# Kernel optimization log

Measured on AMD Instinct MI355X. Metric: run time of the kernel, lower is better.

The kernel has to match this reference:

```python
import jax, jax.numpy as jnp
import numpy as np
from math import sqrt

N_HEADS = 16

def setup_inputs() -> dict:
    key = jax.random.key(0)
    ks = jax.random.split(key, 6)
    B, T, C = 4, 2048, 1024
    s = 0.02
    return {
        "X": jax.random.normal(ks[0], (B, T, C), jnp.float32),
        "Wq": jax.random.normal(ks[1], (C, C), jnp.float32) * s,
        "Wk": jax.random.normal(ks[2], (C, C), jnp.float32) * s,
        "Wv": jax.random.normal(ks[3], (C, C), jnp.float32) * s,
        "Wo": jax.random.normal(ks[4], (C, C), jnp.float32) * s,
        "bo": jnp.zeros((C,), jnp.float32),
    }

def reference(X, Wq, Wk, Wv, Wo, bo):
    B, T, C = X.shape
    H = N_HEADS
    D = C // H
    scale = sqrt(C / H)  # == sqrt(D)
    # Linear layers (torch Linear: y = x @ W.T), split into heads: [B,H,T,D]
    Q = (X @ Wq.T).reshape(B, T, H, D).transpose(0, 2, 1, 3)
    K = (X @ Wk.T).reshape(B, T, H, D).transpose(0, 2, 1, 3)
    V = (X @ Wv.T).reshape(B, T, H, D).transpose(0, 2, 1, 3)
    A = jnp.einsum("bhtd,bhsd->bhts", Q, K) / scale  # [B,H,T,T]
    causal = jnp.tril(jnp.ones((T, T), dtype=bool))
    A = jnp.where(causal, A, -jnp.inf)
    A = jax.nn.softmax(A, axis=-1)
    Y = jnp.einsum("bhts,bhsd->bhtd", A, V)  # [B,H,T,D]
    Y = Y.transpose(0, 2, 1, 3).reshape(B, T, C)
    return Y @ Wo.T + bo
```

## Files before the change

### kernel.cpp

```cpp
#include <hip/hip_runtime.h>
#include <hip/hip_bf16.h>
#include <stdint.h>


typedef unsigned short u16;
typedef __attribute__((ext_vector_type(8))) __bf16 bf16x8;
typedef __attribute__((ext_vector_type(4))) float  f32x4;
typedef __attribute__((ext_vector_type(4))) unsigned short u16x4;
typedef __attribute__((ext_vector_type(4))) short s16x4;

#define B_  4
#define T_  2048
#define C_  1024
#define H_  16
#define D_  64
#define BT_ (B_ * T_)

#define Q_SCALE 0.1803368801111204f

__device__ __forceinline__ u16 f32_to_bf16(float f) {
    unsigned int u = __float_as_uint(f);
    unsigned int r = (u + 0x7FFFu + ((u >> 16) & 1u)) >> 16;
    return (u16)r;
}

__device__ __forceinline__ unsigned int pk_bf16(float a, float b) {
    float2 f2; f2.x = a; f2.y = b;
    __hip_bfloat162 h = __float22bfloat162_rn(f2);
    return *(unsigned int*)&h;
}

__device__ __forceinline__ void async16(const void* g, void* lds) {
    __builtin_amdgcn_global_load_lds(
        (const __attribute__((address_space(1))) void*)g,
        (__attribute__((address_space(3))) void*)lds, 16, 0, 0);
}

__global__ void cast_bf16_kernel(const float* __restrict__ in, u16* __restrict__ out, int n4) {
    int i = blockIdx.x * 256 + threadIdx.x;
    if (i >= n4) return;
    float4 v = ((const float4*)in)[i];
    u16x4 o;
    o[0] = f32_to_bf16(v.x); o[1] = f32_to_bf16(v.y);
    o[2] = f32_to_bf16(v.z); o[3] = f32_to_bf16(v.w);
    ((u16x4*)out)[i] = o;
}

__global__ void cast_w4_kernel(const float* __restrict__ w0, const float* __restrict__ w1,
                               const float* __restrict__ w2, const float* __restrict__ w3,
                               u16* __restrict__ o0, u16* __restrict__ o1,
                               u16* __restrict__ o2, u16* __restrict__ o3) {
    int which = blockIdx.y;
    const float* in = (which == 0) ? w0 : (which == 1) ? w1 : (which == 2) ? w2 : w3;
    u16* out = (which == 0) ? o0 : (which == 1) ? o1 : (which == 2) ? o2 : o3;
    int i = blockIdx.x * 256 + threadIdx.x;
    float4 v = ((const float4*)in)[i];
    u16x4 o;
    o[0] = f32_to_bf16(v.x); o[1] = f32_to_bf16(v.y);
    o[2] = f32_to_bf16(v.z); o[3] = f32_to_bf16(v.w);
    ((u16x4*)out)[i] = o;
}

__device__ __forceinline__ void gemm_core_128(
    const u16* __restrict__ A, const u16* __restrict__ B,
    u16* As, u16* Bs, int m0, int n0, f32x4 (&acc)[4][4])
{
    const int K = C_;
    int tid  = threadIdx.x;
    int lane = tid & 63, w = tid >> 6;
    int quad = lane >> 4, l15 = lane & 15;
    int wm = w >> 1, wn = w & 1;

    int c0 = tid, c1 = tid + 256;
    int row0 = c0 >> 2, row1 = c1 >> 2;
    int gc0 = (((c0 & 3) - (row0 >> 1)) & 3) * 8;
    int gc1 = (((c1 & 3) - (row1 >> 1)) & 3) * 8;
    int ldsb0 = (w * 64) * 16;
    int ldsb1 = (256 + w * 64) * 16;

    const u16* Arow0 = A + (m0 + row0) * K + gc0;
    const u16* Arow1 = A + (m0 + row1) * K + gc1;
    const u16* Brow0 = B + (n0 + row0) * K + gc0;
    const u16* Brow1 = B + (n0 + row1) * K + gc1;

    for (int kt = 0; kt < K / 32; ++kt) {
        int k0 = kt * 32;
        async16(Arow0 + k0, (char*)As + ldsb0);
        async16(Arow1 + k0, (char*)As + ldsb1);
        async16(Brow0 + k0, (char*)Bs + ldsb0);
        async16(Brow1 + k0, (char*)Bs + ldsb1);
        __syncthreads();

        bf16x8 a[4], b[4];
#pragma unroll
        for (int i = 0; i < 4; ++i) {
            int rA = wm * 64 + i * 16 + l15;
            a[i] = *(const bf16x8*)&As[rA * 32 + (((rA >> 1) + quad) & 3) * 8];
            int rB = wn * 64 + i * 16 + l15;
            b[i] = *(const bf16x8*)&Bs[rB * 32 + (((rB >> 1) + quad) & 3) * 8];
        }
#pragma unroll
        for (int i = 0; i < 4; ++i)
#pragma unroll
            for (int j = 0; j < 4; ++j)
                acc[i][j] = __builtin_amdgcn_mfma_f32_16x16x32_bf16(a[i], b[j], acc[i][j], 0, 0, 0);
        __syncthreads();
    }
}

__global__ __launch_bounds__(256, 4) void qkv_gemm(
    const u16* __restrict__ Xb,
    const u16* __restrict__ Wqb, const u16* __restrict__ Wkb, const u16* __restrict__ Wvb,
    u16* __restrict__ Qb, u16* __restrict__ Kb, u16* __restrict__ Vtb)
{
    __shared__ u16 As[128 * 32];
    __shared__ u16 Bs[128 * 32];
    int which = blockIdx.z;
    const u16* W = (which == 0) ? Wqb : ((which == 1) ? Wkb : Wvb);

    f32x4 acc[4][4];
    const f32x4 z4 = {0.f, 0.f, 0.f, 0.f};
#pragma unroll
    for (int i = 0; i < 4; ++i)
#pragma unroll
        for (int j = 0; j < 4; ++j) acc[i][j] = z4;

    int lane = threadIdx.x & 63, w = threadIdx.x >> 6;
    int quad = lane >> 4, l15 = lane & 15;
    int wm = w >> 1, wn = w & 1;

    if (which <= 1) {
        int m0 = blockIdx.x * 128, n0 = blockIdx.y * 128;
        gemm_core_128(W, Xb, As, Bs, m0, n0, acc);
        float s = (which == 0) ? Q_SCALE : 1.0f;
        u16* Out = (which == 0) ? Qb : Kb;
#pragma unroll
        for (int i = 0; i < 4; ++i) {
            int ch0 = m0 + wm * 64 + i * 16 + quad * 4;
#pragma unroll
            for (int j = 0; j < 4; ++j) {
                int t = n0 + wn * 64 + j * 16 + l15;
                u16x4 v;
#pragma unroll
                for (int r = 0; r < 4; ++r) v[r] = f32_to_bf16(acc[i][j][r] * s);
                *(u16x4*)&Out[(size_t)t * C_ + ch0] = v;
            }
        }
    } else {
        int m0 = blockIdx.y * 128, n0 = blockIdx.x * 128;
        gemm_core_128(Xb, W, As, Bs, m0, n0, acc);
#pragma unroll
        for (int i = 0; i < 4; ++i) {
            int t0 = m0 + wm * 64 + i * 16 + quad * 4;
#pragma unroll
            for (int j = 0; j < 4; ++j) {
                int col = n0 + wn * 64 + j * 16 + l15;
                int h = col >> 6, d = col & 63;
                u16x4 v;
#pragma unroll
                for (int r = 0; r < 4; ++r) v[r] = f32_to_bf16(acc[i][j][r]);
                int b = t0 >> 11, t = t0 & (T_ - 1);
                *(u16x4*)&Vtb[(((b * H_ + h) * D_ + d) * T_) + t] = v;
            }
        }
    }
}

__global__ __launch_bounds__(256) void attn_kernel(
    const u16* __restrict__ Qb, const u16* __restrict__ Kb,
    const u16* __restrict__ Vtb, u16* __restrict__ Yb)
{
    __shared__ u16 Ks0[64 * 64], Ks1[64 * 64];
    __shared__ u16 Vs0[64 * 64], Vs1[64 * 64];

    int id = blockIdx.x;
    int kk = id >> 8;
    int cc = id & 255;
    int jj = cc >> 6;
    int bh = cc & 63;
    int qt = (kk == 0) ? jj : (kk == 1) ? (15 - jj) : (kk == 2) ? (jj + 4) : (11 - jj);

    int tid = threadIdx.x, lane = tid & 63, w = tid >> 6;
    int quad = lane >> 4, l15 = lane & 15;
    int qbase = qt * 128;
    int b = bh >> 4, h = bh & 15;

    bf16x8 qf[2][2];
    {
        const u16* q0 = Qb + ((size_t)(b * T_ + qbase + w * 32 + l15)) * C_ + h * 64;
        qf[0][0] = *(const bf16x8*)(q0 + quad * 8);
        qf[0][1] = *(const bf16x8*)(q0 + 32 + quad * 8);
        const u16* q1 = q0 + 16 * C_;
        qf[1][0] = *(const bf16x8*)(q1 + quad * 8);
        qf[1][1] = *(const bf16x8*)(q1 + 32 + quad * 8);
    }

    int koff0[4], koff1[4], voff[4][4];
#pragma unroll
    for (int sblk = 0; sblk < 4; ++sblk) {
        int sr = sblk * 16 + l15;
        koff0[sblk] = (sr * 64 + ((quad + sr) & 7) * 8) * 2;
        koff1[sblk] = (sr * 64 + ((4 + quad + sr) & 7) * 8) * 2;
    }
#pragma unroll
    for (int n = 0; n < 4; ++n)
#pragma unroll
        for (int sblk = 0; sblk < 4; ++sblk) {
            int dr = n * 16 + l15;
            voff[n][sblk] = (dr * 64 + ((sblk * 2 + (quad >> 1) + dr) & 7) * 8 + (quad & 1) * 4) * 2;
        }

    float l_part[2] = {0.f, 0.f};
    f32x4 o_acc[2][4];
    const f32x4 z4 = {0.f, 0.f, 0.f, 0.f};
#pragma unroll
    for (int c = 0; c < 2; ++c)
#pragma unroll
        for (int n = 0; n < 4; ++n) o_acc[c][n] = z4;

    int cA = tid, cB = tid + 256;
    int sA = cA >> 3, sB = cB >> 3;
    int offA = (((cA & 7) - sA) & 7) * 8;
    int offB = (((cB & 7) - sB) & 7) * 8;
    const u16* Kbase = Kb + (size_t)(b * T_) * C_ + h * 64;
    const u16* Vbase = Vtb + (size_t)bh * D_ * T_;
    int ldsb0 = (w * 64) * 16, ldsb1 = (256 + w * 64) * 16;

    const int nst = 2 * qt + 2;

    const u16* kgpA = Kbase + (size_t)sA * C_ + offA;
    const u16* kgpB = Kbase + (size_t)sB * C_ + offB;
    const u16* vgpA = Vbase + sA * T_ + offA;
    const u16* vgpB = Vbase + sB * T_ + offB;

    async16(kgpA, (char*)Ks0 + ldsb0);
    async16(kgpB, (char*)Ks0 + ldsb1);
    async16(vgpA, (char*)Vs0 + ldsb0);
    async16(vgpB, (char*)Vs0 + ldsb1);
    kgpA += 64 * C_; kgpB += 64 * C_; vgpA += 64; vgpB += 64;

    auto tile_body = [&](int st, const u16* K_, const u16* V_, char* Kpf, char* Vpf) {
        __syncthreads();
        if (st + 1 < nst) {
            async16(kgpA, Kpf + ldsb0);
            async16(kgpB, Kpf + ldsb1);
            async16(vgpA, Vpf + ldsb0);
            async16(vgpB, Vpf + ldsb1);
        }
        kgpA += 64 * C_; kgpB += 64 * C_; vgpA += 64; vgpB += 64;

        f32x4 sv[2][4];
#pragma unroll
        for (int sblk = 0; sblk < 4; ++sblk) {
            bf16x8 k0 = *(const bf16x8*)((const char*)K_ + koff0[sblk]);
            bf16x8 k1 = *(const bf16x8*)((const char*)K_ + koff1[sblk]);
#pragma unroll
            for (int c = 0; c < 2; ++c) {
                f32x4 t0 = __builtin_amdgcn_mfma_f32_16x16x32_bf16(k0, qf[c][0], z4, 0, 0, 0);
                sv[c][sblk] = __builtin_amdgcn_mfma_f32_16x16x32_bf16(k1, qf[c][1], t0, 0, 0, 0);
            }
        }

        if (st >= 2 * qt) {
            int sb0 = st * 64 - qbase;
#pragma unroll
            for (int c = 0; c < 2; ++c) {
                int tl = w * 32 + c * 16 + l15;
#pragma unroll
                for (int sblk = 0; sblk < 4; ++sblk)
#pragma unroll
                    for (int r = 0; r < 4; ++r)
                        if (sb0 + sblk * 16 + quad * 4 + r > tl) sv[c][sblk][r] = -1e30f;
            }
        }

        s16x4 pfrag[2][4];
#pragma unroll
        for (int c = 0; c < 2; ++c) {
            f32x4 s4 = z4;
#pragma unroll
            for (int sblk = 0; sblk < 4; ++sblk) {
#pragma unroll
                for (int r = 0; r < 4; ++r)
                    sv[c][sblk][r] = __builtin_amdgcn_exp2f(sv[c][sblk][r]);
                s4 += sv[c][sblk];
                uint2 pk;
                pk.x = pk_bf16(sv[c][sblk][0], sv[c][sblk][1]);
                pk.y = pk_bf16(sv[c][sblk][2], sv[c][sblk][3]);
                pfrag[c][sblk] = *(s16x4*)&pk;
            }
            l_part[c] += (s4[0] + s4[1]) + (s4[2] + s4[3]);
        }

#pragma unroll
        for (int n = 0; n < 4; ++n)
#pragma unroll
            for (int sblk = 0; sblk < 4; ++sblk) {
                s16x4 va = *(const s16x4*)((const char*)V_ + voff[n][sblk]);
#pragma unroll
                for (int c = 0; c < 2; ++c)
                    o_acc[c][n] = __builtin_amdgcn_mfma_f32_16x16x16bf16_1k(va, pfrag[c][sblk], o_acc[c][n], 0, 0, 0);
            }
    };

    for (int st = 0; st < nst; st += 2) {
        tile_body(st,     Ks0, Vs0, (char*)Ks1, (char*)Vs1);
        tile_body(st + 1, Ks1, Vs1, (char*)Ks0, (char*)Vs0);
    }

#pragma unroll
    for (int c = 0; c < 2; ++c) {
        float l = l_part[c];
        l += __shfl_xor(l, 16, 64);
        l += __shfl_xor(l, 32, 64);
        float inv = 1.0f / l;
        int t = qbase + w * 32 + c * 16 + l15;
        size_t rowoff = ((size_t)b * T_ + t) * C_ + h * 64;
#pragma unroll
        for (int n = 0; n < 4; ++n) {
            uint2 pk;
            pk.x = pk_bf16(o_acc[c][n][0] * inv, o_acc[c][n][1] * inv);
            pk.y = pk_bf16(o_acc[c][n][2] * inv, o_acc[c][n][3] * inv);
            *(uint2*)&Yb[rowoff + n * 16 + quad * 4] = pk;
        }
    }
}

__global__ __launch_bounds__(256, 4) void proj_gemm(
    const u16* __restrict__ Yb, const u16* __restrict__ Wob,
    const float* __restrict__ bo, float* __restrict__ out)
{
    __shared__ u16 As[128 * 32];
    __shared__ u16 Bs[128 * 32];
    int m0 = blockIdx.x * 128, n0 = blockIdx.y * 128;

    f32x4 acc[4][4];
    const f32x4 z4 = {0.f, 0.f, 0.f, 0.f};
#pragma unroll
    for (int i = 0; i < 4; ++i)
#pragma unroll
        for (int j = 0; j < 4; ++j) acc[i][j] = z4;

    gemm_core_128(Wob, Yb, As, Bs, m0, n0, acc);

    int lane = threadIdx.x & 63, w = threadIdx.x >> 6;
    int quad = lane >> 4, l15 = lane & 15;
    int wm = w >> 1, wn = w & 1;

#pragma unroll
    for (int i = 0; i < 4; ++i) {
        int ch0 = m0 + wm * 64 + i * 16 + quad * 4;
        float4 b4 = *(const float4*)&bo[ch0];
#pragma unroll
        for (int j = 0; j < 4; ++j) {
            int t = n0 + wn * 64 + j * 16 + l15;
            float4 o;
            o.x = acc[i][j][0] + b4.x;
            o.y = acc[i][j][1] + b4.y;
            o.z = acc[i][j][2] + b4.z;
            o.w = acc[i][j][3] + b4.w;
            *(float4*)&out[(size_t)t * C_ + ch0] = o;
        }
    }
}

extern "C" void kernel_launch(void* const* d_in, const int* in_sizes, int n_in,
                              void* d_out, int out_size, void* d_ws, size_t ws_size,
                              hipStream_t stream) {
    const float* X  = (const float*)d_in[0];
    const float* Wq = (const float*)d_in[1];
    const float* Wk = (const float*)d_in[2];
    const float* Wv = (const float*)d_in[3];
    const float* Wo = (const float*)d_in[4];
    const float* bo = (const float*)d_in[5];

    char* ws = (char*)d_ws;
    u16* Xb  = (u16*)(ws);
    u16* Wqb = (u16*)(ws + (16u << 20));
    u16* Wkb = (u16*)(ws + (18u << 20));
    u16* Wvb = (u16*)(ws + (20u << 20));
    u16* Wob = (u16*)(ws + (22u << 20));
    u16* Qb  = (u16*)(ws + (24u << 20));
    u16* Kb  = (u16*)(ws + (40u << 20));
    u16* Vtb = (u16*)(ws + (56u << 20));
    u16* Yb  = (u16*)(ws + (72u << 20));

    cast_bf16_kernel<<<(BT_ * C_ / 4) / 256, 256, 0, stream>>>(X, Xb, BT_ * C_ / 4);
    cast_w4_kernel<<<dim3((C_ * C_ / 4) / 256, 4), 256, 0, stream>>>(
        Wq, Wk, Wv, Wo, Wqb, Wkb, Wvb, Wob);

    qkv_gemm<<<dim3(C_ / 128, BT_ / 128, 3), 256, 0, stream>>>(Xb, Wqb, Wkb, Wvb, Qb, Kb, Vtb);
    attn_kernel<<<dim3((T_ / 128) * B_ * H_), 256, 0, stream>>>(Qb, Kb, Vtb, Yb);
    proj_gemm<<<dim3(C_ / 128, BT_ / 128), 256, 0, stream>>>(Yb, Wob, bo, (float*)d_out);
}
```

Before: 264.6 us.

## Double-buffer GEMM LDS tiles and remap blocks for XCD-local reuse

The shared GEMM core now uses two LDS buffers, so the async global-to-LDS loads for the next K tile are issued while MFMAs run on the current tile. This removes one barrier per iteration and lets load latency overlap with compute. The QKV and projection GEMMs also switch to a 1D grid with a custom block-to-tile mapping, so the blocks placed on each XCD share rows of X/Y and get better L2 reuse. The cost is doubled LDS per block, which may lower occupancy, plus extra index arithmetic.

```diff
diff --git a/kernel.cpp b/kernel.cpp
--- a/kernel.cpp
+++ b/kernel.cpp
@@ -61,11 +61,12 @@
     ((u16x4*)out)[i] = o;
 }
 
-__device__ __forceinline__ void gemm_core_128(
+__device__ __forceinline__ void gemm_core_128_db(
     const u16* __restrict__ A, const u16* __restrict__ B,
     u16* As, u16* Bs, int m0, int n0, f32x4 (&acc)[4][4])
 {
     const int K = C_;
+    const int KT = K / 32;
     int tid  = threadIdx.x;
     int lane = tid & 63, w = tid >> 6;
     int quad = lane >> 4, l15 = lane & 15;
@@ -78,33 +79,51 @@
     int ldsb0 = (w * 64) * 16;
     int ldsb1 = (256 + w * 64) * 16;
 
-    const u16* Arow0 = A + (m0 + row0) * K + gc0;
-    const u16* Arow1 = A + (m0 + row1) * K + gc1;
-    const u16* Brow0 = B + (n0 + row0) * K + gc0;
-    const u16* Brow1 = B + (n0 + row1) * K + gc1;
-
-    for (int kt = 0; kt < K / 32; ++kt) {
-        int k0 = kt * 32;
-        async16(Arow0 + k0, (char*)As + ldsb0);
-        async16(Arow1 + k0, (char*)As + ldsb1);
-        async16(Brow0 + k0, (char*)Bs + ldsb0);
-        async16(Brow1 + k0, (char*)Bs + ldsb1);
+    const u16* ApA = A + (size_t)(m0 + row0) * K + gc0;
+    const u16* ApB = A + (size_t)(m0 + row1) * K + gc1;
+    const u16* BpA = B + (size_t)(n0 + row0) * K + gc0;
+    const u16* BpB = B + (size_t)(n0 + row1) * K + gc1;
+
+    char* As0 = (char*)As; char* As1 = (char*)As + 8192;
+    char* Bs0 = (char*)Bs; char* Bs1 = (char*)Bs + 8192;
+
+    int aoff[4], boff[4];
+#pragma unroll
+    for (int i = 0; i < 4; ++i) {
+        int rA = wm * 64 + i * 16 + l15;
+        aoff[i] = (rA * 32 + (((rA >> 1) + quad) & 3) * 8) * 2;
+        int rB = wn * 64 + i * 16 + l15;
+        boff[i] = (rB * 32 + (((rB >> 1) + quad) & 3) * 8) * 2;
+    }
+
+    async16(ApA, As0 + ldsb0); async16(ApB, As0 + ldsb1);
+    async16(BpA, Bs0 + ldsb0); async16(BpB, Bs0 + ldsb1);
+    ApA += 32; ApB += 32; BpA += 32; BpB += 32;
+
+    auto body = [&](int kt, const char* Ac, const char* Bc, char* Apf, char* Bpf) {
         __syncthreads();
+        if (kt + 1 < KT) {
+            async16(ApA, Apf + ldsb0); async16(ApB, Apf + ldsb1);
+            async16(BpA, Bpf + ldsb0); async16(BpB, Bpf + ldsb1);
+        }
+        ApA += 32; ApB += 32; BpA += 32; BpB += 32;
 
         bf16x8 a[4], b[4];
 #pragma unroll
         for (int i = 0; i < 4; ++i) {
-            int rA = wm * 64 + i * 16 + l15;
-            a[i] = *(const bf16x8*)&As[rA * 32 + (((rA >> 1) + quad) & 3) * 8];
-            int rB = wn * 64 + i * 16 + l15;
-            b[i] = *(const bf16x8*)&Bs[rB * 32 + (((rB >> 1) + quad) & 3) * 8];
+            a[i] = *(const bf16x8*)(Ac + aoff[i]);
+            b[i] = *(const bf16x8*)(Bc + boff[i]);
         }
 #pragma unroll
         for (int i = 0; i < 4; ++i)
 #pragma unroll
             for (int j = 0; j < 4; ++j)
                 acc[i][j] = __builtin_amdgcn_mfma_f32_16x16x32_bf16(a[i], b[j], acc[i][j], 0, 0, 0);
-        __syncthreads();
+    };
+
+    for (int kt = 0; kt < KT; kt += 2) {
+        body(kt,     As0, Bs0, As1, Bs1);
+        body(kt + 1, As1, Bs1, As0, Bs0);
     }
 }
 
@@ -113,9 +132,18 @@
     const u16* __restrict__ Wqb, const u16* __restrict__ Wkb, const u16* __restrict__ Wvb,
     u16* __restrict__ Qb, u16* __restrict__ Kb, u16* __restrict__ Vtb)
 {
-    __shared__ u16 As[128 * 32];
-    __shared__ u16 Bs[128 * 32];
-    int which = blockIdx.z;
+    __shared__ u16 As[2 * 128 * 32];
+    __shared__ u16 Bs[2 * 128 * 32];
+
+    int id = blockIdx.x;
+    int xcd = id & 7;
+    int local = id >> 3;
+    int yloc = local & 7;
+    int zx = local >> 3;
+    int bx = zx & 7;
+    int which = zx >> 3;
+    int by = xcd * 8 + yloc;
+
     const u16* W = (which == 0) ? Wqb : ((which == 1) ? Wkb : Wvb);
 
     f32x4 acc[4][4];
@@ -130,8 +158,8 @@
     int wm = w >> 1, wn = w & 1;
 
     if (which <= 1) {
-        int m0 = blockIdx.x * 128, n0 = blockIdx.y * 128;
-        gemm_core_128(W, Xb, As, Bs, m0, n0, acc);
+        int m0 = bx * 128, n0 = by * 128;
+        gemm_core_128_db(W, Xb, As, Bs, m0, n0, acc);
         float s = (which == 0) ? Q_SCALE : 1.0f;
         u16* Out = (which == 0) ? Qb : Kb;
 #pragma unroll
@@ -147,8 +175,8 @@
             }
         }
     } else {
-        int m0 = blockIdx.y * 128, n0 = blockIdx.x * 128;
-        gemm_core_128(Xb, W, As, Bs, m0, n0, acc);
+        int m0 = by * 128, n0 = bx * 128;
+        gemm_core_128_db(Xb, W, As, Bs, m0, n0, acc);
 #pragma unroll
         for (int i = 0; i < 4; ++i) {
             int t0 = m0 + wm * 64 + i * 16 + quad * 4;
@@ -330,9 +358,15 @@
     const u16* __restrict__ Yb, const u16* __restrict__ Wob,
     const float* __restrict__ bo, float* __restrict__ out)
 {
-    __shared__ u16 As[128 * 32];
-    __shared__ u16 Bs[128 * 32];
-    int m0 = blockIdx.x * 128, n0 = blockIdx.y * 128;
+    __shared__ u16 As[2 * 128 * 32];
+    __shared__ u16 Bs[2 * 128 * 32];
+
+    int id = blockIdx.x;
+    int xcd = id & 7;
+    int local = id >> 3;
+    int by = xcd * 8 + (local & 7);
+    int bx = local >> 3;
+    int m0 = bx * 128, n0 = by * 128;
 
     f32x4 acc[4][4];
     const f32x4 z4 = {0.f, 0.f, 0.f, 0.f};
@@ -341,7 +375,7 @@
 #pragma unroll
         for (int j = 0; j < 4; ++j) acc[i][j] = z4;
 
-    gemm_core_128(Wob, Yb, As, Bs, m0, n0, acc);
+    gemm_core_128_db(Wob, Yb, As, Bs, m0, n0, acc);
 
     int lane = threadIdx.x & 63, w = threadIdx.x >> 6;
     int quad = lane >> 4, l15 = lane & 15;
@@ -389,7 +423,7 @@
     cast_w4_kernel<<<dim3((C_ * C_ / 4) / 256, 4), 256, 0, stream>>>(
         Wq, Wk, Wv, Wo, Wqb, Wkb, Wvb, Wob);
 
-    qkv_gemm<<<dim3(C_ / 128, BT_ / 128, 3), 256, 0, stream>>>(Xb, Wqb, Wkb, Wvb, Qb, Kb, Vtb);
+    qkv_gemm<<<dim3(3 * 8 * 64), 256, 0, stream>>>(Xb, Wqb, Wkb, Wvb, Qb, Kb, Vtb);
     attn_kernel<<<dim3((T_ / 128) * B_ * H_), 256, 0, stream>>>(Qb, Kb, Vtb, Yb);
-    proj_gemm<<<dim3(C_ / 128, BT_ / 128), 256, 0, stream>>>(Yb, Wob, bo, (float*)d_out);
-}
+    proj_gemm<<<dim3(8 * 64), 256, 0, stream>>>(Yb, Wob, bo, (float*)d_out);
+}
```

Result: slower. 278.8 us (+5.4%).
